# Kernel tuning notes

Measured on AMD Instinct MI355X. Metric: run time of the kernel, lower is better.

The kernel has to match this reference:

```python
import jax, jax.numpy as jnp
import numpy as np

IN_DIMS = (8, 8, 8, 8)
OUT_DIMS = (8, 8, 8, 8)
RANKS = (1, 16, 16, 16, 1)
BATCH = 4096


def setup_inputs() -> dict:
    key = jax.random.key(0)
    ks = jax.random.split(key, 6)
    n_in = int(np.prod(IN_DIMS))
    n_out = int(np.prod(OUT_DIMS))
    d = len(IN_DIMS)
    # t3f glorot: total matrix variance 2/(n_in+n_out), split evenly across cores/ranks
    lamb = 2.0 / (n_in + n_out)
    cv = (lamb / np.prod(RANKS)) ** (1.0 / d)
    core_std = float(np.sqrt(cv))
    cores = {}
    for i in range(d):
        shp = (RANKS[i], IN_DIMS[i], OUT_DIMS[i], RANKS[i + 1])
        cores[f"core{i}"] = core_std * jax.random.normal(ks[i], shp, dtype=jnp.float32)
    x = jax.random.normal(ks[4], (BATCH, n_in), dtype=jnp.float32)
    b = 0.1 * jnp.ones((n_out,), dtype=jnp.float32)
    return {"x": x, **cores, "b": b}


def tt_dense(x, cores):
    """y = x @ M, M the TT-matrix with cores [r_{k-1}, a_k, b_k, r_k]."""
    B = x.shape[0]
    rest = int(np.prod(IN_DIMS[1:]))
    # t: [B, P(out dims done), r, a_k, rest(in dims todo)]
    t = x.reshape(B, 1, 1, IN_DIMS[0], rest)
    for k, core in enumerate(cores):
        # contract rank r and input mode a_k -> produce output mode b_k and next rank q
        t = jnp.einsum('zpras,rabq->zpbqs', t, core)
        z, p, bd, q, s = t.shape
        if k < len(cores) - 1:
            a_next = IN_DIMS[k + 1]
            t = t.reshape(z, p * bd, q, a_next, s // a_next)
        else:
            t = t.reshape(z, p * bd)  # q == s == 1
    return t  # [B, prod(OUT_DIMS)]


def reference(x, core0, core1, core2, core3, b):
    y = tt_dense(x, [core0, core1, core2, core3])
    return jax.nn.relu(y + b)
```

## Files before the change

kernel.cpp:

```cpp
#include <hip/hip_runtime.h>
#include <hip/hip_bf16.h>
#include <cstdint>
#include <cstddef>


#define GM 4096
#define GN 4096
#define GK 4096
#define NT (GK / 64)

typedef __attribute__((ext_vector_type(8))) short short8_t;
typedef __attribute__((ext_vector_type(4))) float float4_t;

__device__ __forceinline__ unsigned short f2bf(float f) {
  union { float f; uint32_t u; } v; v.f = f;
  uint32_t u = v.u;
  uint32_t r = (u + 0x7fffu + ((u >> 16) & 1u)) >> 16;
  return (unsigned short)r;
}

__global__ __launch_bounds__(256) void prep_kernel(
    const float* __restrict__ c0, const float* __restrict__ c1,
    const float* __restrict__ c2, const float* __restrict__ c3,
    float* __restrict__ G01, float* __restrict__ G23t) {
  int idx = blockIdx.x * 256 + threadIdx.x;
  if (idx < 65536) {
    int r2 = idx & 15;
    int b01 = (idx >> 4) & 63;
    int a01 = idx >> 10;
    int a0 = a01 >> 3, a1 = a01 & 7, b0 = b01 >> 3, b1 = b01 & 7;
    float s = 0.f;
#pragma unroll
    for (int r1 = 0; r1 < 16; ++r1)
      s += c0[(a0 * 8 + b0) * 16 + r1] * c1[((r1 * 8 + a1) * 8 + b1) * 16 + r2];
    G01[idx] = s;
  } else {
    int t = idx - 65536;
    int a23 = t & 63;
    int b23 = (t >> 6) & 63;
    int r2 = t >> 12;
    int a2 = a23 >> 3, a3 = a23 & 7, b2 = b23 >> 3, b3 = b23 & 7;
    float s = 0.f;
#pragma unroll
    for (int r3 = 0; r3 < 16; ++r3)
      s += c2[((r2 * 8 + a2) * 8 + b2) * 16 + r3] * c3[(r3 * 8 + a3) * 8 + b3];
    G23t[t] = s;
  }
}

__global__ __launch_bounds__(256) void mt_convert(
    const float* __restrict__ G01, const float* __restrict__ G23t,
    unsigned short* __restrict__ Mt,
    const float* __restrict__ x, unsigned short* __restrict__ xb) {
  int bid = blockIdx.x;
  int tid = threadIdx.x;
  if (bid < 1024) {
    int a01 = bid >> 4;
    int g = bid & 15;

    float acc[4][16];
#pragma unroll
    for (int j = 0; j < 4; ++j)
#pragma unroll
      for (int i = 0; i < 16; ++i) acc[j][i] = 0.f;

    for (int r2 = 0; r2 < 16; ++r2) {
      float gv[4];
#pragma unroll
      for (int j = 0; j < 4; ++j)
        gv[j] = G01[(a01 * 64 + g * 4 + j) * 16 + r2];
      const float* src = G23t + r2 * 4096 + tid * 16;
      float4_t v0 = *(const float4_t*)(src);
      float4_t v1 = *(const float4_t*)(src + 4);
      float4_t v2 = *(const float4_t*)(src + 8);
      float4_t v3 = *(const float4_t*)(src + 12);
#pragma unroll
      for (int j = 0; j < 4; ++j) {
#pragma unroll
        for (int l = 0; l < 4; ++l) {
          acc[j][l]      += gv[j] * v0[l];
          acc[j][4 + l]  += gv[j] * v1[l];
          acc[j][8 + l]  += gv[j] * v2[l];
          acc[j][12 + l] += gv[j] * v3[l];
        }
      }
    }

    int b23 = tid >> 2;
    int a23base = (tid & 3) * 16;
#pragma unroll
    for (int j = 0; j < 4; ++j) {
      short8_t o0, o1;
#pragma unroll
      for (int i = 0; i < 8; ++i) {
        o0[i] = (short)f2bf(acc[j][i]);
        o1[i] = (short)f2bf(acc[j][8 + i]);
      }
      size_t base = (size_t)((g * 4 + j) * 64 + b23) * GK + a01 * 64 + a23base;
      *(short8_t*)(Mt + base) = o0;
      *(short8_t*)(Mt + base + 8) = o1;
    }
  } else {
    int i = ((bid - 1024) * 256 + tid) * 8;
    float4_t a = *(const float4_t*)(x + i);
    float4_t b = *(const float4_t*)(x + i + 4);
    short8_t o;
    o[0] = (short)f2bf(a[0]); o[1] = (short)f2bf(a[1]);
    o[2] = (short)f2bf(a[2]); o[3] = (short)f2bf(a[3]);
    o[4] = (short)f2bf(b[0]); o[5] = (short)f2bf(b[1]);
    o[6] = (short)f2bf(b[2]); o[7] = (short)f2bf(b[3]);
    *(short8_t*)(xb + i) = o;
  }
}

__global__ __launch_bounds__(512, 2) void gemm_bias_relu(
    const unsigned short* __restrict__ A, const unsigned short* __restrict__ Bt,
    const float* __restrict__ bias, float* __restrict__ C) {
  extern __shared__ __align__(16) unsigned short lds[];

  const int tid = threadIdx.x;
  const int bswz = blockIdx.x;
  const int xcd = bswz & 7, li = bswz >> 3;
  const int row0 = ((xcd >> 1) * 4 + (li >> 3)) * 256;
  const int col0 = ((xcd & 1) * 8 + (li & 7)) * 256;
  const int wave = tid >> 6, lane = tid & 63;
  const int wm = wave >> 2, wn = wave & 3;
  const int half = lane >> 4, mrow = lane & 15;

  const int r0 = tid >> 3, p0 = tid & 7, h0 = (p0 - r0) & 7;
  const unsigned short* Abase = A + (size_t)(row0 + r0) * GK + h0 * 8;
  const unsigned short* Bbase = Bt + (size_t)(col0 + r0) * GK + h0 * 8;
  const int dA = r0 * 64 + p0 * 8;
  const int dB = dA + 16384;

#define GLD(SRC, DST)                                                  \
  __builtin_amdgcn_global_load_lds(                                    \
      (const __attribute__((address_space(1))) void*)(SRC),            \
      (__attribute__((address_space(3))) void*)(lds + (DST)), 16, 0, 0)
#define STAGE_A(G, KT, BUF)                                            \
  do {                                                                 \
    const unsigned short* s_ = Abase + (size_t)(G) * 128 * GK + (KT) * 64; \
    GLD(s_, (BUF) * 32768 + (G) * 8192 + dA);                          \
    GLD(s_ + (size_t)64 * GK, (BUF) * 32768 + (G) * 8192 + dA + 4096); \
  } while (0)
#define STAGE_B(G, KT, BUF)                                            \
  do {                                                                 \
    const unsigned short* s_ = Bbase + (size_t)(G) * 128 * GK + (KT) * 64; \
    GLD(s_, (BUF) * 32768 + (G) * 8192 + dB);                          \
    GLD(s_ + (size_t)64 * GK, (BUF) * 32768 + (G) * 8192 + dB + 4096); \
  } while (0)

  const int arow = wm * 128 + mrow;
  const int aoff0 = arow * 64 + ((half + arow) & 7) * 8;
  const int aoff1 = aoff0 ^ 32;
  const int brow = wn * 64 + mrow;
  const int boff0 = 16384 + brow * 64 + ((half + brow) & 7) * 8;
  const int boff1 = boff0 ^ 32;

#define RD_AH(DST, BUF, MT0)                                                \
  do {                                                                      \
    _Pragma("unroll")                                                       \
    for (int m = 0; m < 4; ++m) {                                           \
      DST[m * 2 + 0] =                                                      \
          *(const short8_t*)&lds[(BUF)*32768 + aoff0 + ((MT0) + m) * 1024]; \
      DST[m * 2 + 1] =                                                      \
          *(const short8_t*)&lds[(BUF)*32768 + aoff1 + ((MT0) + m) * 1024]; \
    }                                                                       \
  } while (0)
#define RD_BH(DST, BUF, NT0)                                                \
  do {                                                                      \
    _Pragma("unroll")                                                       \
    for (int n = 0; n < 2; ++n) {                                           \
      DST[n * 2 + 0] =                                                      \
          *(const short8_t*)&lds[(BUF)*32768 + boff0 + ((NT0) + n) * 1024]; \
      DST[n * 2 + 1] =                                                      \
          *(const short8_t*)&lds[(BUF)*32768 + boff1 + ((NT0) + n) * 1024]; \
    }                                                                       \
  } while (0)
#define MFMA_H(MB, AF, NB, BF)                                              \
  do {                                                                      \
    _Pragma("unroll")                                                       \
    for (int ks = 0; ks < 2; ++ks)                                          \
      _Pragma("unroll")                                                     \
      for (int m = 0; m < 4; ++m)                                           \
        _Pragma("unroll")                                                   \
        for (int n = 0; n < 2; ++n)                                         \
          acc[(MB) + m][(NB) + n] = __builtin_amdgcn_mfma_f32_16x16x32_bf16(\
              AF[m * 2 + ks], BF[n * 2 + ks], acc[(MB) + m][(NB) + n],      \
              0, 0, 0);                                                     \
  } while (0)

#define TILE(CB, OB, KT)                                                    \
  do {                                                                      \
                                                 \
    RD_AH(a0f, CB, 0);                                                      \
    RD_BH(b0f, CB, 0);                                                      \
    if ((KT) + 1 < NT) STAGE_B(1, (KT) + 1, OB);                            \
    __builtin_amdgcn_s_barrier();                                           \
    MFMA_H(0, a0f, 0, b0f);                                                 \
    __builtin_amdgcn_s_barrier();                                           \
      \
    RD_BH(b1f, CB, 2);                                                      \
    MFMA_H(0, a0f, 2, b1f);                                                 \
    asm volatile("s_waitcnt lgkmcnt(0)" ::: "memory");                      \
    __builtin_amdgcn_s_barrier();                                           \
                 \
    RD_AH(a1f, CB, 4);                                                      \
    if ((KT) + 2 < NT) STAGE_B(0, (KT) + 2, CB);                            \
    MFMA_H(4, a1f, 2, b1f);                                                 \
    asm volatile("s_waitcnt lgkmcnt(0)" ::: "memory");                      \
    __builtin_amdgcn_s_barrier();                                           \
          \
    if ((KT) + 2 < NT) { STAGE_A(0, (KT) + 2, CB); STAGE_A(1, (KT) + 2, CB); } \
    MFMA_H(4, a1f, 0, b0f);                                                 \
    if ((KT) + 2 < NT)                                                      \
      asm volatile("s_waitcnt vmcnt(6)" ::: "memory");                      \
    else if ((KT) + 1 < NT)                                                 \
      asm volatile("s_waitcnt vmcnt(0)" ::: "memory");                      \
    __builtin_amdgcn_s_barrier();                                           \
    __builtin_amdgcn_sched_barrier(0);                                      \
  } while (0)

  float4_t acc[8][4];
#pragma unroll
  for (int i = 0; i < 8; ++i)
#pragma unroll
    for (int n = 0; n < 4; ++n) acc[i][n] = (float4_t){0.f, 0.f, 0.f, 0.f};

  short8_t a0f[8], a1f[8], b0f[4], b1f[4];

  STAGE_A(0, 0, 0); STAGE_A(1, 0, 0); STAGE_B(0, 0, 0); STAGE_B(1, 0, 0);
  STAGE_B(0, 1, 1); STAGE_A(0, 1, 1); STAGE_A(1, 1, 1);
  asm volatile("s_waitcnt vmcnt(6)" ::: "memory");
  __builtin_amdgcn_s_barrier();
  __builtin_amdgcn_sched_barrier(0);

  for (int kt = 0; kt < NT; kt += 2) {
    TILE(0, 1, kt);
    TILE(1, 0, kt + 1);
  }

#undef TILE
#undef MFMA_H
#undef RD_BH
#undef RD_AH
#undef STAGE_B
#undef STAGE_A
#undef GLD

#pragma unroll
  for (int n = 0; n < 4; ++n) {
    int col = col0 + wn * 64 + n * 16 + mrow;
    float bcol = bias[col];
#pragma unroll
    for (int i = 0; i < 8; ++i) {
#pragma unroll
      for (int r = 0; r < 4; ++r) {
        int row = row0 + wm * 128 + i * 16 + half * 4 + r;
        float v = acc[i][n][r] + bcol;
        C[(size_t)row * GN + col] = v > 0.f ? v : 0.f;
      }
    }
  }
}

extern "C" void kernel_launch(void* const* d_in, const int* in_sizes, int n_in,
                              void* d_out, int out_size, void* d_ws, size_t ws_size,
                              hipStream_t stream) {
  const float* x  = (const float*)d_in[0];
  const float* c0 = (const float*)d_in[1];
  const float* c1 = (const float*)d_in[2];
  const float* c2 = (const float*)d_in[3];
  const float* c3 = (const float*)d_in[4];
  const float* b  = (const float*)d_in[5];
  float* out = (float*)d_out;

  unsigned short* xb = (unsigned short*)d_ws;
  unsigned short* Mt = (unsigned short*)((char*)d_ws + (32u << 20));
  float* G01 = (float*)((char*)d_ws + (64u << 20));
  float* G23t = G01 + 65536;

  static bool lds_configured = false;
  if (!lds_configured) {
    (void)hipFuncSetAttribute((const void*)gemm_bias_relu,
                              hipFuncAttributeMaxDynamicSharedMemorySize,
                              131072);
    lds_configured = true;
  }

  prep_kernel<<<512, 256, 0, stream>>>(c0, c1, c2, c3, G01, G23t);
  mt_convert<<<1024 + (GM * GK) / (256 * 8), 256, 0, stream>>>(
      G01, G23t, Mt, x, xb);
  gemm_bias_relu<<<(GM / 256) * (GN / 256), 512, 131072, stream>>>(
      xb, Mt, b, out);
}
```

Measured before the change: 248.7 us.

## Fuse prep, convert and GEMM into one persistent kernel with grid barriers

Merges the three launches (core contraction, TT-matrix/x bf16 conversion, GEMM) into a single 256-block kernel that uses a software sense-reversing grid barrier between phases. This removes two kernel launch gaps and tail effects between kernels. It depends on all 256 blocks being co-resident (2 per CU at 128KB LDS). It also adds barrier spin overhead and puts the x conversion onto the same 256 blocks instead of a wide grid.

```diff
diff --git a/kernel.cpp b/kernel.cpp
--- a/kernel.cpp
+++ b/kernel.cpp
@@ -8,6 +8,8 @@
 #define GN 4096
 #define GK 4096
 #define NT (GK / 64)
+#define NBLK 256
+#define BAR_MAGIC 0x0123456789ABCDEFull
 
 typedef __attribute__((ext_vector_type(8))) short short8_t;
 typedef __attribute__((ext_vector_type(4))) float float4_t;
@@ -19,107 +21,172 @@
   return (unsigned short)r;
 }
 
-__global__ __launch_bounds__(256) void prep_kernel(
+struct __align__(16) GridBar {
+  unsigned long long flag;
+  unsigned count;
+  unsigned sense;
+};
+
+__device__ __forceinline__ void gbar(GridBar* gb, unsigned* ls) {
+  while (__hip_atomic_load(&gb->flag, __ATOMIC_ACQUIRE,
+                           __HIP_MEMORY_SCOPE_AGENT) != BAR_MAGIC)
+    __builtin_amdgcn_s_sleep(1);
+  unsigned target = *ls ^ 1u;
+  __threadfence();
+  unsigned prev = __hip_atomic_fetch_add(&gb->count, 1u, __ATOMIC_ACQ_REL,
+                                         __HIP_MEMORY_SCOPE_AGENT);
+  if (prev == NBLK - 1) {
+    __hip_atomic_store(&gb->count, 0u, __ATOMIC_RELAXED,
+                       __HIP_MEMORY_SCOPE_AGENT);
+    __hip_atomic_store(&gb->sense, target, __ATOMIC_RELEASE,
+                       __HIP_MEMORY_SCOPE_AGENT);
+  } else {
+    while (__hip_atomic_load(&gb->sense, __ATOMIC_ACQUIRE,
+                             __HIP_MEMORY_SCOPE_AGENT) != target)
+      __builtin_amdgcn_s_sleep(1);
+  }
+  __threadfence();
+  *ls = target;
+}
+
+__global__ __launch_bounds__(512, 2) void tt_fused(
+    const float* __restrict__ x,
     const float* __restrict__ c0, const float* __restrict__ c1,
     const float* __restrict__ c2, const float* __restrict__ c3,
-    float* __restrict__ G01, float* __restrict__ G23t) {
-  int idx = blockIdx.x * 256 + threadIdx.x;
-  if (idx < 65536) {
-    int r2 = idx & 15;
-    int b01 = (idx >> 4) & 63;
-    int a01 = idx >> 10;
-    int a0 = a01 >> 3, a1 = a01 & 7, b0 = b01 >> 3, b1 = b01 & 7;
-    float s = 0.f;
-#pragma unroll
-    for (int r1 = 0; r1 < 16; ++r1)
-      s += c0[(a0 * 8 + b0) * 16 + r1] * c1[((r1 * 8 + a1) * 8 + b1) * 16 + r2];
-    G01[idx] = s;
-  } else {
-    int t = idx - 65536;
-    int a23 = t & 63;
-    int b23 = (t >> 6) & 63;
-    int r2 = t >> 12;
-    int a2 = a23 >> 3, a3 = a23 & 7, b2 = b23 >> 3, b3 = b23 & 7;
-    float s = 0.f;
-#pragma unroll
-    for (int r3 = 0; r3 < 16; ++r3)
-      s += c2[((r2 * 8 + a2) * 8 + b2) * 16 + r3] * c3[(r3 * 8 + a3) * 8 + b3];
-    G23t[t] = s;
-  }
-}
-
-__global__ __launch_bounds__(256) void mt_convert(
-    const float* __restrict__ G01, const float* __restrict__ G23t,
-    unsigned short* __restrict__ Mt,
-    const float* __restrict__ x, unsigned short* __restrict__ xb) {
-  int bid = blockIdx.x;
-  int tid = threadIdx.x;
-  if (bid < 1024) {
-    int a01 = bid >> 4;
-    int g = bid & 15;
-
-    float acc[4][16];
-#pragma unroll
-    for (int j = 0; j < 4; ++j)
-#pragma unroll
-      for (int i = 0; i < 16; ++i) acc[j][i] = 0.f;
-
-    for (int r2 = 0; r2 < 16; ++r2) {
-      float gv[4];
+    const float* __restrict__ bias, float* __restrict__ out,
+    unsigned short* __restrict__ xb, unsigned short* __restrict__ Mt,
+    float* __restrict__ G01, float* __restrict__ G23t, GridBar* gb) {
+  extern __shared__ __align__(16) unsigned short lds[];
+
+  const int tid = threadIdx.x;
+  const int bid = blockIdx.x;
+
+  if (bid == 0 && tid == 0) {
+    if (__hip_atomic_load(&gb->flag, __ATOMIC_RELAXED,
+                          __HIP_MEMORY_SCOPE_AGENT) != BAR_MAGIC) {
+      __hip_atomic_store(&gb->count, 0u, __ATOMIC_RELAXED,
+                         __HIP_MEMORY_SCOPE_AGENT);
+      __hip_atomic_store(&gb->sense, 0u, __ATOMIC_RELAXED,
+                         __HIP_MEMORY_SCOPE_AGENT);
+      __hip_atomic_store(&gb->flag, BAR_MAGIC, __ATOMIC_RELEASE,
+                         __HIP_MEMORY_SCOPE_AGENT);
+    }
+  }
+  unsigned lsense = 0;
+
+  {
+    int idx = bid * 512 + tid;
+    if (idx < 65536) {
+      int r2 = idx & 15;
+      int b01 = (idx >> 4) & 63;
+      int a01 = idx >> 10;
+      int a0 = a01 >> 3, a1 = a01 & 7, b0 = b01 >> 3, b1 = b01 & 7;
+      float s = 0.f;
+#pragma unroll
+      for (int r1 = 0; r1 < 16; ++r1)
+        s += c0[(a0 * 8 + b0) * 16 + r1] *
+             c1[((r1 * 8 + a1) * 8 + b1) * 16 + r2];
+      G01[idx] = s;
+    } else {
+      int t = idx - 65536;
+      int a23 = t & 63;
+      int b23 = (t >> 6) & 63;
+      int r2 = t >> 12;
+      int a2 = a23 >> 3, a3 = a23 & 7, b2 = b23 >> 3, b3 = b23 & 7;
+      float s = 0.f;
+#pragma unroll
+      for (int r3 = 0; r3 < 16; ++r3)
+        s += c2[((r2 * 8 + a2) * 8 + b2) * 16 + r3] *
+             c3[(r3 * 8 + a3) * 8 + b3];
+      G23t[t] = s;
+    }
+  }
+
+  __threadfence();
+  __syncthreads();
+  if (tid == 0) gbar(gb, &lsense);
+  __syncthreads();
+
+  {
+    const int sub = tid >> 8;
+    const int stid = tid & 255;
+    for (int it = 0; it < 2; ++it) {
+      const int ob = bid * 4 + it * 2 + sub;
+      const int a01 = ob >> 4;
+      const int g = ob & 15;
+
+      float acc2[4][16];
 #pragma unroll
       for (int j = 0; j < 4; ++j)
-        gv[j] = G01[(a01 * 64 + g * 4 + j) * 16 + r2];
-      const float* src = G23t + r2 * 4096 + tid * 16;
-      float4_t v0 = *(const float4_t*)(src);
-      float4_t v1 = *(const float4_t*)(src + 4);
-      float4_t v2 = *(const float4_t*)(src + 8);
-      float4_t v3 = *(const float4_t*)(src + 12);
-#pragma unroll
-      for (int j = 0; j < 4; ++j) {
-#pragma unroll
-        for (int l = 0; l < 4; ++l) {
-          acc[j][l]      += gv[j] * v0[l];
-          acc[j][4 + l]  += gv[j] * v1[l];
-          acc[j][8 + l]  += gv[j] * v2[l];
-          acc[j][12 + l] += gv[j] * v3[l];
+#pragma unroll
+        for (int i = 0; i < 16; ++i) acc2[j][i] = 0.f;
+
+      for (int r2 = 0; r2 < 16; ++r2) {
+        float gv[4];
+#pragma unroll
+        for (int j = 0; j < 4; ++j)
+          gv[j] = G01[(a01 * 64 + g * 4 + j) * 16 + r2];
+        const float* src = G23t + r2 * 4096 + stid * 16;
+        float4_t v0 = *(const float4_t*)(src);
+        float4_t v1 = *(const float4_t*)(src + 4);
+        float4_t v2 = *(const float4_t*)(src + 8);
+        float4_t v3 = *(const float4_t*)(src + 12);
+#pragma unroll
+        for (int j = 0; j < 4; ++j) {
+#pragma unroll
+          for (int l = 0; l < 4; ++l) {
+            acc2[j][l]      += gv[j] * v0[l];
+            acc2[j][4 + l]  += gv[j] * v1[l];
+            acc2[j][8 + l]  += gv[j] * v2[l];
+            acc2[j][12 + l] += gv[j] * v3[l];
+          }
         }
       }
-    }
-
-    int b23 = tid >> 2;
-    int a23base = (tid & 3) * 16;
-#pragma unroll
-    for (int j = 0; j < 4; ++j) {
-      short8_t o0, o1;
-#pragma unroll
-      for (int i = 0; i < 8; ++i) {
-        o0[i] = (short)f2bf(acc[j][i]);
-        o1[i] = (short)f2bf(acc[j][8 + i]);
+
+      int b23 = stid >> 2;
+      int a23base = (stid & 3) * 16;
+#pragma unroll
+      for (int j = 0; j < 4; ++j) {
+        short8_t o0, o1;
+#pragma unroll
+        for (int i = 0; i < 8; ++i) {
+          o0[i] = (short)f2bf(acc2[j][i]);
+          o1[i] = (short)f2bf(acc2[j][8 + i]);
+        }
+        size_t base =
+            (size_t)((g * 4 + j) * 64 + b23) * GK + a01 * 64 + a23base;
+        *(short8_t*)(Mt + base) = o0;
+        *(short8_t*)(Mt + base + 8) = o1;
       }
-      size_t base = (size_t)((g * 4 + j) * 64 + b23) * GK + a01 * 64 + a23base;
-      *(short8_t*)(Mt + base) = o0;
-      *(short8_t*)(Mt + base + 8) = o1;
-    }
-  } else {
-    int i = ((bid - 1024) * 256 + tid) * 8;
-    float4_t a = *(const float4_t*)(x + i);
-    float4_t b = *(const float4_t*)(x + i + 4);
-    short8_t o;
-    o[0] = (short)f2bf(a[0]); o[1] = (short)f2bf(a[1]);
-    o[2] = (short)f2bf(a[2]); o[3] = (short)f2bf(a[3]);
-    o[4] = (short)f2bf(b[0]); o[5] = (short)f2bf(b[1]);
-    o[6] = (short)f2bf(b[2]); o[7] = (short)f2bf(b[3]);
-    *(short8_t*)(xb + i) = o;
-  }
-}
-
-__global__ __launch_bounds__(512, 2) void gemm_bias_relu(
-    const unsigned short* __restrict__ A, const unsigned short* __restrict__ Bt,
-    const float* __restrict__ bias, float* __restrict__ C) {
-  extern __shared__ __align__(16) unsigned short lds[];
-
-  const int tid = threadIdx.x;
-  const int bswz = blockIdx.x;
+    }
+  }
+
+  {
+    const int gtid = bid * 512 + tid;
+#pragma unroll 4
+    for (int it = 0; it < 16; ++it) {
+      int i = (it * 131072 + gtid) * 8;
+      float4_t av = *(const float4_t*)(x + i);
+      float4_t bv = *(const float4_t*)(x + i + 4);
+      short8_t o;
+      o[0] = (short)f2bf(av[0]); o[1] = (short)f2bf(av[1]);
+      o[2] = (short)f2bf(av[2]); o[3] = (short)f2bf(av[3]);
+      o[4] = (short)f2bf(bv[0]); o[5] = (short)f2bf(bv[1]);
+      o[6] = (short)f2bf(bv[2]); o[7] = (short)f2bf(bv[3]);
+      *(short8_t*)(xb + i) = o;
+    }
+  }
+
+  __threadfence();
+  __syncthreads();
+  if (tid == 0) gbar(gb, &lsense);
+  __syncthreads();
+  __builtin_amdgcn_sched_barrier(0);
+
+  const unsigned short* A = xb;
+  const unsigned short* Bt = Mt;
+
+  const int bswz = bid;
   const int xcd = bswz & 7, li = bswz >> 3;
   const int row0 = ((xcd >> 1) * 4 + (li >> 3)) * 256;
   const int col0 = ((xcd & 1) * 8 + (li & 7)) * 256;
@@ -258,7 +325,7 @@
       for (int r = 0; r < 4; ++r) {
         int row = row0 + wm * 128 + i * 16 + half * 4 + r;
         float v = acc[i][n][r] + bcol;
-        C[(size_t)row * GN + col] = v > 0.f ? v : 0.f;
+        out[(size_t)row * GN + col] = v > 0.f ? v : 0.f;
       }
     }
   }
@@ -279,18 +346,16 @@
   unsigned short* Mt = (unsigned short*)((char*)d_ws + (32u << 20));
   float* G01 = (float*)((char*)d_ws + (64u << 20));
   float* G23t = G01 + 65536;
+  GridBar* gb = (GridBar*)((char*)d_ws + (64u << 20) + (512u << 10));
 
   static bool lds_configured = false;
   if (!lds_configured) {
-    (void)hipFuncSetAttribute((const void*)gemm_bias_relu,
+    (void)hipFuncSetAttribute((const void*)tt_fused,
                               hipFuncAttributeMaxDynamicSharedMemorySize,
                               131072);
     lds_configured = true;
   }
 
-  prep_kernel<<<512, 256, 0, stream>>>(c0, c1, c2, c3, G01, G23t);
-  mt_convert<<<1024 + (GM * GK) / (256 * 8), 256, 0, stream>>>(
-      G01, G23t, Mt, x, xb);
-  gemm_bias_relu<<<(GM / 256) * (GN / 256), 512, 131072, stream>>>(
-      xb, Mt, b, out);
+  tt_fused<<<NBLK, 512, 131072, stream>>>(x, c0, c1, c2, c3, b, out,
+                                          xb, Mt, G01, G23t, gb);
 }
```

Measured after the change: 466.2 us. 87.5% more time.
